# Kernel optimization log

Hardware: AMD Instinct MI355X
Metric: run time of the kernel (lower is better)

The kernel has to match this reference:

```python
import jax, jax.numpy as jnp
import numpy as np

N_ATOMS = 10000
N_PAIRS = 320000
C = 64        # channel width (pp_nodes[-1], ii_nodes[-1], pi_nodes[-1])
NB = 10       # n_basis
EPS = 1e-3    # torsion-boost epsilon


def setup_inputs() -> dict:
    key = jax.random.key(0)
    ks = jax.random.split(key, 24)
    f32 = jnp.float32

    def w(k, shp):
        return jax.random.normal(k, shp, f32) / np.float32(np.sqrt(shp[0]))

    ind_2 = jax.random.randint(ks[0], (N_PAIRS, 2), 0, N_ATOMS)
    p1 = jax.random.normal(ks[1], (N_ATOMS, C), f32)
    p3 = jax.random.normal(ks[2], (N_ATOMS, 3, C), f32)
    basis = jax.random.uniform(ks[3], (N_PAIRS, NB), dtype=f32)
    d3 = jax.random.normal(ks[4], (N_PAIRS, 3), f32)
    d3 = d3 / jnp.linalg.norm(d3, axis=-1, keepdims=True)  # unit bond directions
    fc_edge = jax.random.uniform(ks[5], (N_PAIRS, 1), dtype=f32)  # cutoff in [0,1]

    return {
        'ind_2': ind_2, 'p1': p1, 'p3': p3, 'basis': basis, 'd3': d3, 'fc_edge': fc_edge,
        'pp_pre_W1': w(ks[6], (C, C)), 'pp_pre_b1': jnp.zeros((C,), f32),
        'pp_pre_W2': w(ks[7], (C, C)), 'pp_pre_b2': jnp.zeros((C,), f32),
        'pi_W': w(ks[8], (2 * C, C * NB)), 'pi_b': jnp.zeros((C * NB,), f32),
        'ii_W': w(ks[9], (C, 2 * C)),
        'pp_post_W1': w(ks[10], (2 * C, C)), 'pp_post_W2': w(ks[11], (C, C)),
        'eq_pp_W': w(ks[12], (C, C)),
        'pp1_W1': w(ks[13], (2 * C, C)), 'pp1_b1': jnp.zeros((C,), f32),
        'pp1_W2': w(ks[14], (C, 2 * C)), 'pp1_b2': jnp.zeros((2 * C,), f32),
    }


def _gc_block(ind_2, p1, p3, basis, d3, fc_edge,
              pp_pre_W1, pp_pre_b1, pp_pre_W2, pp_pre_b2,
              pi_W, pi_b, ii_W, pp_post_W1, pp_post_W2,
              eq_pp_W, pp1_W1, pp1_b1, pp1_W2, pp1_b2):
    n_atoms = p1.shape[0]
    i = ind_2[:, 0]
    j = ind_2[:, 1]

    # ---- InvarLayer ----
    # pp_pre: FF [C,C], tanh, bias
    p1_in = jnp.tanh(jnp.tanh(p1 @ pp_pre_W1 + pp_pre_b1) @ pp_pre_W2 + pp_pre_b2)
    # PILayer: concat(p1[i], p1[j]) -> Dense(C*NB) -> contract with radial basis
    pair = jnp.concatenate([p1_in[i], p1_in[j]], axis=-1)            # (P, 2C)
    h = jnp.tanh(pair @ pi_W + pi_b).reshape(-1, C, NB)              # (P, C, NB)
    i_pair = jnp.einsum('pcb,pb->pc', h, basis)                      # (P, C)
    # ii: FF [2C] (doubled for n_props=2), tanh, no bias
    i_pair = jnp.tanh(i_pair @ ii_W)                                 # (P, 2C)
    # IP: scatter-add onto receiver atom i
    p1_scat = jax.ops.segment_sum(i_pair, i, num_segments=n_atoms)   # (N, 2C)
    # pp_post: FF [C,C], tanh, no bias
    p1_new = jnp.tanh(jnp.tanh(p1_scat @ pp_post_W1) @ pp_post_W2)   # (N, C)

    i1a, i1b = jnp.split(i_pair, 2, axis=-1)  # chunks; rank-3 branch uses i1s[1]

    # ---- torsion boost (compute_torsion_boost_t3) ----
    v = jax.ops.segment_sum(d3 * fc_edge, i, num_segments=n_atoms)   # (N, 3)
    v_i = v[i]
    proj = jnp.sum(v_i * d3, axis=-1, keepdims=True)
    w = v_i - proj * d3                                              # perpendicular part
    w2 = jnp.sum(w * w, axis=-1, keepdims=True)
    g_deg = w2 / (w2 + (10.0 * EPS) ** 2)
    t3 = w * jax.lax.rsqrt(w2 + EPS * EPS) * g_deg                   # (P, 3)
    tb_gate = g_deg * (fc_edge * fc_edge)                            # (P, 1)

    # ---- EquivarLayer ----
    gate = i1b[:, None, :]                                           # (P, 1, C)
    ix = p3[j] * gate + d3[:, :, None] * gate \
         + t3[:, :, None] * (i1b * tb_gate)[:, None, :]              # (P, 3, C)
    p3_new = jax.ops.segment_sum(ix, i, num_segments=n_atoms)        # (N, 3, C)
    p3_new = p3_new @ eq_pp_W                                        # PP: no bias, no act
    dotted = jnp.einsum('ixr,ixr->ir', p3_new, p3_new)               # (N, C)

    # ---- output PP + gating ----
    h2 = jnp.tanh(jnp.concatenate([p1_new, dotted], axis=-1) @ pp1_W1 + pp1_b1)
    h2 = jnp.tanh(h2 @ pp1_W2 + pp1_b2)                              # (N, 2C)
    g1, g3 = jnp.split(h2, 2, axis=-1)
    p1_out = g1                                                      # (N, C)
    p3_out = p3_new * g3[:, None, :]                                 # ScaleLayer
    return p1_out, p3_out


def reference(ind_2, p1, p3, basis, d3, fc_edge,
              pp_pre_W1, pp_pre_b1, pp_pre_W2, pp_pre_b2,
              pi_W, pi_b, ii_W, pp_post_W1, pp_post_W2,
              eq_pp_W, pp1_W1, pp1_b1, pp1_W2, pp1_b2):
    return _gc_block(ind_2, p1, p3, basis, d3, fc_edge,
                     pp_pre_W1, pp_pre_b1, pp_pre_W2, pp_pre_b2,
                     pi_W, pi_b, ii_W, pp_post_W1, pp_post_W2,
                     eq_pp_W, pp1_W1, pp1_b1, pp1_W2, pp1_b2)
```

## Files before the change

### kernel.cpp

```cpp
#include <hip/hip_runtime.h>
#include <hip/hip_bf16.h>

#define N_ATOMS 10000
#define N_PAIRS 320000
#define C_ 64
#define NB_ 10

typedef short bf16x8 __attribute__((ext_vector_type(8)));
typedef float f32x4 __attribute__((ext_vector_type(4)));

__device__ __forceinline__ float bf2f(__hip_bfloat16 x) { return __bfloat162float(x); }
__device__ __forceinline__ float ldf(const void* p, int i, int isf32) {
    return isf32 ? ((const float*)p)[i] : bf2f(((const __hip_bfloat16*)p)[i]);
}
__device__ __forceinline__ short f2bs(float x) {
    __hip_bfloat16 h = __float2bfloat16(x);
    return *reinterpret_cast<short*>(&h);
}
__device__ __forceinline__ float bs2f(unsigned short s) {
    return __uint_as_float(((unsigned)s) << 16);
}
__device__ __forceinline__ float tanh_fast(float x) {
    const float e = __expf(2.0f * x);
    return 1.0f - 2.0f * __builtin_amdgcn_rcpf(e + 1.0f);
}

#define W_PPREW1 0
#define W_PPREB1 4096
#define W_PPREW2 4160
#define W_PPREB2 8256
#define W_PIW    8320
#define W_PIB    90240
#define W_IIW    90880
#define W_PPOSTW1 99072
#define W_PPOSTW2 107264
#define W_EQW    111360
#define W_Q1W    115456
#define W_Q1B    123648
#define W_Q2W    123712
#define W_Q2B    131904
#define W_TOTAL  132032

__device__ __forceinline__ int probe_eval(const void* d3)
{
    float sf = 0.f, sb = 0.f;
    const float* f = (const float*)d3;
    const __hip_bfloat16* b = (const __hip_bfloat16*)d3;
    for (int r = 0; r < 4; r++) {
        float x = f[r*3], y = f[r*3+1], z = f[r*3+2];
        float n = x*x + y*y + z*z;
        sf += isfinite(n) ? fabsf(n - 1.f) : 1e30f;
        float xb = bf2f(b[r*3]), yb = bf2f(b[r*3+1]), zb = bf2f(b[r*3+2]);
        float nb = xb*xb + yb*yb + zb*zb;
        sb += isfinite(nb) ? fabsf(nb - 1.f) : 1e30f;
    }
    return (sf < sb) ? 1 : 0;
}

__global__ void k_probe(const void* __restrict__ d3, int* __restrict__ flag)
{
    if (threadIdx.x == 0 && blockIdx.x == 0) *flag = probe_eval(d3);
}

__global__ __launch_bounds__(256) void k_probe_hist_v(
    const void* __restrict__ d3, const void* __restrict__ fc,
    int* __restrict__ flag, const int* __restrict__ ind2,
    int* __restrict__ cnt, float* __restrict__ v)
{
    __shared__ int fsh;
    if (threadIdx.x == 0) {
        const int fv = probe_eval(d3);
        fsh = fv;
        if (blockIdx.x == 0) *flag = fv;
    }
    __syncthreads();
    const int isf32 = fsh;
    const int p = blockIdx.x * 256 + threadIdx.x;
    if (p >= N_PAIRS) return;
    const int ia = ind2[2 * p];
    atomicAdd(&cnt[ia], 1);
    const float f = ldf(fc, p, isf32);
    #pragma unroll
    for (int x = 0; x < 3; x++)
        atomicAdd(&v[ia * 3 + x], ldf(d3, 3 * p + x, isf32) * f);
}

__global__ __launch_bounds__(256) void k_convert_scan(
    const void* s0, const void* s1, const void* s2, const void* s3,
    const void* s4, const void* s5, const void* s6, const void* s7,
    const void* s8, const void* s9, const void* s10, const void* s11,
    const void* s12, const void* s13,
    float* __restrict__ wbuf, const int* __restrict__ flagp,
    const int* __restrict__ cnt, int* __restrict__ offs, int* __restrict__ cur)
{
    __shared__ int part[256];
    __shared__ int base[257];
    if (blockIdx.x < 516) {
        const int idx = blockIdx.x * 256 + threadIdx.x;
        if (idx >= W_TOTAL) return;
        const int isf32 = *flagp;
        const int offw[15] = {W_PPREW1, W_PPREB1, W_PPREW2, W_PPREB2, W_PIW, W_PIB,
                              W_IIW, W_PPOSTW1, W_PPOSTW2, W_EQW, W_Q1W, W_Q1B,
                              W_Q2W, W_Q2B, W_TOTAL};
        const void* srcs[14] = {s0,s1,s2,s3,s4,s5,s6,s7,s8,s9,s10,s11,s12,s13};
        int t = 0;
        while (idx >= offw[t + 1]) t++;
        wbuf[idx] = ldf(srcs[t], idx - offw[t], isf32);
        return;
    }
    const int t = threadIdx.x;
    const int lo = t * 40, hi = (lo + 40 < N_ATOMS) ? lo + 40 : N_ATOMS;
    int s = 0;
    for (int b = lo; b < hi; b++) s += cnt[b];
    part[t] = s;
    __syncthreads();
    if (t == 0) {
        int run = 0;
        for (int i = 0; i < 256; i++) { base[i] = run; run += part[i]; }
        base[256] = run;
    }
    __syncthreads();
    int run = base[t];
    for (int b = lo; b < hi; b++) { offs[b] = run; cur[b] = run; run += cnt[b]; }
    if (t == 0) offs[N_ATOMS] = base[256];
}

__global__ __launch_bounds__(256) void k_prep_scatter(
    const float* __restrict__ wbuf,
    short* __restrict__ piWB2,
    short* __restrict__ iiWh, short* __restrict__ iiWl,
    const void* __restrict__ p1, const int* __restrict__ flagp,
    unsigned short* __restrict__ p1h, unsigned short* __restrict__ p1l,
    const int* __restrict__ ind2, int* __restrict__ cur, int* __restrict__ perm)
{
    __shared__ float x[4][C_];
    __shared__ float h[4][C_];
    if (blockIdx.x >= 2852) {
        const int p = (blockIdx.x - 2852) * 256 + threadIdx.x;
        if (p < N_PAIRS) {
            const int pos = atomicAdd(&cur[ind2[2 * p]], 1);
            perm[pos] = p;
        }
        return;
    }
    if (blockIdx.x < 352) {
        int idx = blockIdx.x * 256 + threadIdx.x;
        if (idx < 81920) {
            const int j = idx & 7, lane = (idx >> 3) & 63, s = (idx >> 9) & 3, T = idx >> 11;
            const int k = s * 32 + (lane >> 4) * 8 + j;
            const int colp = T * 16 + (lane & 15);
            const int b = colp >> 6, c = colp & 63;
            const float v = wbuf[W_PIW + k * 640 + c * 10 + b];
            const short hs = f2bs(v);
            const int cc = idx >> 13, e = idx & 8191;
            piWB2[cc * 16384 + e] = hs;
            piWB2[cc * 16384 + 8192 + e] = f2bs(v - bs2f((unsigned short)hs));
            return;
        }
        idx -= 81920;
        if (idx < 8192) {
            const int j = idx & 7, lane = (idx >> 3) & 63, s2 = (idx >> 9) & 1, ct = idx >> 10;
            const int k = s2 * 32 + (lane >> 4) * 8 + j;
            const int col = ct * 16 + (lane & 15);
            const float wv = wbuf[W_IIW + k * 128 + col];
            const short hs = f2bs(wv);
            iiWh[idx] = hs;
            iiWl[idx] = f2bs(wv - bs2f((unsigned short)hs));
        }
        return;
    }
    const float* W1 = wbuf + W_PPREW1;
    const float* b1 = wbuf + W_PPREB1;
    const float* W2 = wbuf + W_PPREW2;
    const float* b2 = wbuf + W_PPREB2;
    const int isf32 = *flagp;
    const int t = threadIdx.x;
    const int slot = t >> 6, c = t & 63;
    const int atom = (blockIdx.x - 352) * 4 + slot;
    x[slot][c] = ldf(p1, atom * C_ + c, isf32);
    __syncthreads();
    float acc = b1[c];
    for (int k = 0; k < C_; k++) acc += x[slot][k] * W1[k * C_ + c];
    h[slot][c] = tanh_fast(acc);
    __syncthreads();
    acc = b2[c];
    for (int k = 0; k < C_; k++) acc += h[slot][k] * W2[k * C_ + c];
    const float f = tanh_fast(acc);
    const short hs = f2bs(f);
    p1h[atom * C_ + c] = (unsigned short)hs;
    p1l[atom * C_ + c] = (unsigned short)f2bs(f - bs2f((unsigned short)hs));
}

__global__ __launch_bounds__(256) void k_pairs_fused(
    const int* __restrict__ ind2, const void* __restrict__ basis,
    const void* __restrict__ d3, const void* __restrict__ fc,
    const int* __restrict__ perm,
    const void* __restrict__ p3,
    const float* __restrict__ wbuf,
    const short* __restrict__ piWB2,
    const short* __restrict__ iiWh, const short* __restrict__ iiWl,
    const unsigned short* __restrict__ p1h, const unsigned short* __restrict__ p1l,
    const int* __restrict__ flagp, const float* __restrict__ vglob,
    float* __restrict__ p1scat, float* __restrict__ p3acc)
{
    __shared__ __align__(16) char SH[33280];
    __shared__ float basisL[640];
    __shared__ float biasT[640];
    __shared__ int sIL[65], sJL[64];
    __shared__ float d3L[64][3], t3L[64][3], tbL[64];

    unsigned short* Bbuf = (unsigned short*)SH;
    float* preL = (float*)SH;
    float* ipL  = (float*)SH;

    const int t = threadIdx.x;
    const int bid = blockIdx.x;
    const int P0 = ((bid & 7) * 625 + (bid >> 3)) * 64;
    const int isf32 = *flagp;
    const int lane = t & 63;
    const int w = t >> 6;
    const int lc = lane & 15;
    const int quad = lane >> 4;

    if (t < 64) {
        const int p = perm[P0 + t];
        int2 ij = ((const int2*)ind2)[p];
        sIL[t] = ij.x; sJL[t] = ij.y;
        const float vi0 = vglob[ij.x * 3 + 0], vi1 = vglob[ij.x * 3 + 1], vi2 = vglob[ij.x * 3 + 2];
        const float d0 = ldf(d3, 3 * p + 0, isf32);
        const float d1 = ldf(d3, 3 * p + 1, isf32);
        const float d2 = ldf(d3, 3 * p + 2, isf32);
        d3L[t][0] = d0; d3L[t][1] = d1; d3L[t][2] = d2;
        const float proj = vi0 * d0 + vi1 * d1 + vi2 * d2;
        const float w0 = vi0 - proj * d0, w1 = vi1 - proj * d1, w2v = vi2 - proj * d2;
        const float w2 = w0 * w0 + w1 * w1 + w2v * w2v;
        const float g = w2 / (w2 + 1e-4f);
        const float rs = rsqrtf(w2 + 1e-6f);
        t3L[t][0] = w0 * rs * g; t3L[t][1] = w1 * rs * g; t3L[t][2] = w2v * rs * g;
        const float f = ldf(fc, p, isf32);
        tbL[t] = g * f * f;
    }
    if (t == 64) sIL[64] = -1;
    for (int e = t; e < 640; e += 256) {
        const int pm = e / 10, col = e - pm * 10;
        basisL[e] = ldf(basis, perm[P0 + pm] * 10 + col, isf32);
    }
    for (int e = t; e < 640; e += 256) biasT[e] = wbuf[W_PIB + (e & 63) * 10 + (e >> 6)];
    __syncthreads();

    bf16x8 ah[4], al[4];
    {
        const int ia = sIL[w * 16 + lc];
        const int ja = sJL[w * 16 + lc];
        #pragma unroll
        for (int s = 0; s < 4; s++) {
            const int atom = (s < 2) ? ia : ja;
            const int off = atom * 64 + (s & 1) * 32 + quad * 8;
            ah[s] = *(const bf16x8*)(p1h + off);
            al[s] = *(const bf16x8*)(p1l + off);
        }
    }

    float sr[4][4];
    #pragma unroll
    for (int r = 0; r < 4; r++)
        #pragma unroll
        for (int ph = 0; ph < 4; ph++) sr[r][ph] = 0.f;

    for (int cc = 0; cc < 10; cc++) {
        if (cc) __syncthreads();
        {
            const uint4* gsrc = (const uint4*)(piWB2 + cc * 16384);
            uint4* ldst = (uint4*)Bbuf;
            #pragma unroll
            for (int r = 0; r < 8; r++) ldst[r * 256 + t] = gsrc[r * 256 + t];
        }
        __syncthreads();
        #pragma unroll
        for (int tt = 0; tt < 4; tt++) {
            f32x4 acc = {0.f, 0.f, 0.f, 0.f};
            #pragma unroll
            for (int s = 0; s < 4; s++) {
                const int e = ((tt * 4 + s) * 64 + lane) * 8;
                bf16x8 bh = *(const bf16x8*)&Bbuf[e];
                bf16x8 bl = *(const bf16x8*)&Bbuf[8192 + e];
                acc = __builtin_amdgcn_mfma_f32_16x16x32_bf16(ah[s], bh, acc, 0, 0, 0);
                acc = __builtin_amdgcn_mfma_f32_16x16x32_bf16(al[s], bh, acc, 0, 0, 0);
                acc = __builtin_amdgcn_mfma_f32_16x16x32_bf16(ah[s], bl, acc, 0, 0, 0);
            }
            const float bias = biasT[cc * 64 + tt * 16 + lc];
            #pragma unroll
            for (int r = 0; r < 4; r++) {
                const int m = w * 16 + quad * 4 + r;
                const float h = tanh_fast(acc[r] + bias);
                sr[r][tt] += h * basisL[m * 10 + cc];
            }
        }
    }
    __syncthreads();

    #pragma unroll
    for (int r = 0; r < 4; r++)
        #pragma unroll
        for (int ph = 0; ph < 4; ph++)
            preL[(w * 16 + quad * 4 + r) * 68 + ph * 16 + lc] = sr[r][ph];
    __syncthreads();

    bf16x8 ah2[2], al2[2];
    {
        const int row = w * 16 + lc;
        #pragma unroll
        for (int s2 = 0; s2 < 2; s2++) {
            const float* pr2 = &preL[row * 68 + s2 * 32 + quad * 8];
            #pragma unroll
            for (int j = 0; j < 8; j++) {
                const float x = pr2[j];
                const short hs = f2bs(x);
                ah2[s2][j] = hs;
                al2[s2][j] = f2bs(x - bs2f((unsigned short)hs));
            }
        }
    }
    __syncthreads();

    float pv0[16];
    if (t < 192) {
        #pragma unroll
        for (int u = 0; u < 16; u++) pv0[u] = ldf(p3, sJL[u] * 192 + t, isf32);
    }

    #pragma unroll
    for (int ct = 0; ct < 8; ct++) {
        f32x4 acc = {0.f, 0.f, 0.f, 0.f};
        #pragma unroll
        for (int s2 = 0; s2 < 2; s2++) {
            bf16x8 bh = *(const bf16x8*)&iiWh[((ct * 2 + s2) * 64 + lane) * 8];
            bf16x8 bl = *(const bf16x8*)&iiWl[((ct * 2 + s2) * 64 + lane) * 8];
            acc = __builtin_amdgcn_mfma_f32_16x16x32_bf16(ah2[s2], bh, acc, 0, 0, 0);
            acc = __builtin_amdgcn_mfma_f32_16x16x32_bf16(al2[s2], bh, acc, 0, 0, 0);
            acc = __builtin_amdgcn_mfma_f32_16x16x32_bf16(ah2[s2], bl, acc, 0, 0, 0);
        }
        const int ch = ct * 16 + lc;
        #pragma unroll
        for (int r = 0; r < 4; r++) {
            const int m = w * 16 + quad * 4 + r;
            ipL[m * 130 + ch] = tanh_fast(acc[r]);
        }
    }
    __syncthreads();

    if (t < 192) {
        const int x = t >> 6, cc2 = t & 63;
        float acc = 0.f;
        #pragma unroll
        for (int blk = 0; blk < 4; blk++) {
            float pv[16];
            if (blk == 0) {
                #pragma unroll
                for (int u = 0; u < 16; u++) pv[u] = pv0[u];
            } else {
                #pragma unroll
                for (int u = 0; u < 16; u++)
                    pv[u] = ldf(p3, sJL[blk * 16 + u] * 192 + t, isf32);
            }
            #pragma unroll
            for (int u = 0; u < 16; u++) {
                const int m = blk * 16 + u;
                const float ipb = ipL[m * 130 + 64 + cc2];
                acc += (pv[u] + d3L[m][x]) * ipb + t3L[m][x] * (ipb * tbL[m]);
                if (sIL[m + 1] != sIL[m]) {
                    atomicAdd(&p3acc[(size_t)sIL[m] * 192 + t], acc);
                    acc = 0.f;
                }
            }
        }
    } else {
        const int ch0 = t - 192;
        float a0 = 0.f, a1 = 0.f;
        #pragma unroll 8
        for (int m = 0; m < 64; m++) {
            a0 += ipL[m * 130 + ch0];
            a1 += ipL[m * 130 + 64 + ch0];
            if (sIL[m + 1] != sIL[m]) {
                const size_t base = (size_t)sIL[m] * 128;
                atomicAdd(&p1scat[base + ch0], a0);
                atomicAdd(&p1scat[base + 64 + ch0], a1);
                a0 = 0.f; a1 = 0.f;
            }
        }
    }
}

__global__ __launch_bounds__(256) void k_pairs_atomic(
    const int* __restrict__ ind2, const void* __restrict__ basis,
    const void* __restrict__ d3, const void* __restrict__ fc,
    const void* __restrict__ p3,
    const float* __restrict__ wbuf,
    const short* __restrict__ piWB2,
    const short* __restrict__ iiWh, const short* __restrict__ iiWl,
    const unsigned short* __restrict__ p1h, const unsigned short* __restrict__ p1l,
    const int* __restrict__ flagp, const float* __restrict__ vglob,
    float* __restrict__ outA, float* __restrict__ outB)
{
    __shared__ __align__(16) unsigned short Bbuf[8192];
    __shared__ __align__(16) char SH[17408];
    __shared__ float basisL[640];
    __shared__ int sIL[64], sJL[64];
    __shared__ float d3L[64][3], t3L[64][3], tbL[64];

    float* preL = (float*)SH;
    float* i1bL = (float*)SH;

    const int t = threadIdx.x;
    const int P0 = blockIdx.x * 64;
    const int isf32 = *flagp;
    const int lane = t & 63;
    const int w = t >> 6;
    const int lc = lane & 15;
    const int quad = lane >> 4;

    if (t < 64) {
        int2 ij = ((const int2*)ind2)[P0 + t];
        sIL[t] = ij.x; sJL[t] = ij.y;
    }
    for (int e = t; e < 640; e += 256) basisL[e] = ldf(basis, P0 * 10 + e, isf32);
    __syncthreads();

    bf16x8 ah[4], al[4];
    {
        const int ia = sIL[w * 16 + lc];
        const int ja = sJL[w * 16 + lc];
        #pragma unroll
        for (int s = 0; s < 4; s++) {
            const int atom = (s < 2) ? ia : ja;
            const int off = atom * 64 + (s & 1) * 32 + quad * 8;
            ah[s] = *(const bf16x8*)(p1h + off);
            al[s] = *(const bf16x8*)(p1l + off);
        }
    }

    float sr[4][4];
    #pragma unroll
    for (int r = 0; r < 4; r++)
        #pragma unroll
        for (int ph = 0; ph < 4; ph++) sr[r][ph] = 0.f;

    for (int cc = 0; cc < 10; cc++) {
        f32x4 acc[4];
        #pragma unroll
        for (int tt = 0; tt < 4; tt++) acc[tt] = (f32x4){0.f, 0.f, 0.f, 0.f};

        __syncthreads();
        {
            const uint4* gsrc = (const uint4*)(piWB2 + cc * 16384);
            uint4* ldst = (uint4*)Bbuf;
            #pragma unroll
            for (int r = 0; r < 4; r++) ldst[r * 256 + t] = gsrc[r * 256 + t];
        }
        __syncthreads();
        #pragma unroll
        for (int tt = 0; tt < 4; tt++) {
            #pragma unroll
            for (int s = 0; s < 4; s++) {
                bf16x8 bfr = *(const bf16x8*)&Bbuf[((tt * 4 + s) * 64 + lane) * 8];
                acc[tt] = __builtin_amdgcn_mfma_f32_16x16x32_bf16(ah[s], bfr, acc[tt], 0, 0, 0);
                acc[tt] = __builtin_amdgcn_mfma_f32_16x16x32_bf16(al[s], bfr, acc[tt], 0, 0, 0);
            }
        }
        __syncthreads();
        {
            const uint4* gsrc = (const uint4*)(piWB2 + cc * 16384 + 8192);
            uint4* ldst = (uint4*)Bbuf;
            #pragma unroll
            for (int r = 0; r < 4; r++) ldst[r * 256 + t] = gsrc[r * 256 + t];
        }
        __syncthreads();
        #pragma unroll
        for (int tt = 0; tt < 4; tt++) {
            #pragma unroll
            for (int s = 0; s < 4; s++) {
                bf16x8 bfr = *(const bf16x8*)&Bbuf[((tt * 4 + s) * 64 + lane) * 8];
                acc[tt] = __builtin_amdgcn_mfma_f32_16x16x32_bf16(ah[s], bfr, acc[tt], 0, 0, 0);
            }
            const int c = tt * 16 + lc;
            const float bias = wbuf[W_PIB + c * 10 + cc];
            #pragma unroll
            for (int r = 0; r < 4; r++) {
                const int m = w * 16 + quad * 4 + r;
                const float h = tanh_fast(acc[tt][r] + bias);
                sr[r][tt] += h * basisL[m * 10 + cc];
            }
        }
    }

    #pragma unroll
    for (int r = 0; r < 4; r++)
        #pragma unroll
        for (int ph = 0; ph < 4; ph++)
            preL[(w * 16 + quad * 4 + r) * 68 + ph * 16 + lc] = sr[r][ph];
    __syncthreads();

    bf16x8 ah2[2], al2[2];
    {
        const int row = w * 16 + lc;
        #pragma unroll
        for (int s2 = 0; s2 < 2; s2++) {
            const float* pr2 = &preL[row * 68 + s2 * 32 + quad * 8];
            #pragma unroll
            for (int j = 0; j < 8; j++) {
                const float x = pr2[j];
                const short hs = f2bs(x);
                ah2[s2][j] = hs;
                al2[s2][j] = f2bs(x - bs2f((unsigned short)hs));
            }
        }
    }
    __syncthreads();

    #pragma unroll
    for (int ct = 0; ct < 8; ct++) {
        f32x4 acc = {0.f, 0.f, 0.f, 0.f};
        #pragma unroll
        for (int s2 = 0; s2 < 2; s2++) {
            bf16x8 bh = *(const bf16x8*)&iiWh[((ct * 2 + s2) * 64 + lane) * 8];
            bf16x8 bl = *(const bf16x8*)&iiWl[((ct * 2 + s2) * 64 + lane) * 8];
            acc = __builtin_amdgcn_mfma_f32_16x16x32_bf16(ah2[s2], bh, acc, 0, 0, 0);
            acc = __builtin_amdgcn_mfma_f32_16x16x32_bf16(al2[s2], bh, acc, 0, 0, 0);
            acc = __builtin_amdgcn_mfma_f32_16x16x32_bf16(ah2[s2], bl, acc, 0, 0, 0);
        }
        const int ch = ct * 16 + lc;
        #pragma unroll
        for (int r = 0; r < 4; r++) {
            const int m = w * 16 + quad * 4 + r;
            const float val = tanh_fast(acc[r]);
            atomicAdd(&outA[(size_t)sIL[m] * 128 + ch], val);
            if (ch >= 64) i1bL[m * 64 + (ch - 64)] = val;
        }
    }

    __syncthreads();
    if (t < 64) {
        const int m = t;
        const int ia = sIL[m];
        const float vi0 = vglob[ia * 3 + 0], vi1 = vglob[ia * 3 + 1], vi2 = vglob[ia * 3 + 2];
        const float d0 = ldf(d3, (P0 + m) * 3 + 0, isf32);
        const float d1 = ldf(d3, (P0 + m) * 3 + 1, isf32);
        const float d2 = ldf(d3, (P0 + m) * 3 + 2, isf32);
        d3L[m][0] = d0; d3L[m][1] = d1; d3L[m][2] = d2;
        const float proj = vi0 * d0 + vi1 * d1 + vi2 * d2;
        const float w0 = vi0 - proj * d0, w1 = vi1 - proj * d1, w2v = vi2 - proj * d2;
        const float w2 = w0 * w0 + w1 * w1 + w2v * w2v;
        const float g = w2 / (w2 + 1e-4f);
        const float rs = rsqrtf(w2 + 1e-6f);
        t3L[m][0] = w0 * rs * g; t3L[m][1] = w1 * rs * g; t3L[m][2] = w2v * rs * g;
        const float f = ldf(fc, P0 + m, isf32);
        tbL[m] = g * f * f;
    }
    __syncthreads();
    const int c = lane;
    #pragma unroll 4
    for (int mm = 0; mm < 16; mm++) {
        const int m = w * 16 + mm;
        const float bv = i1bL[m * 64 + c];
        const float coef = bv * tbL[m];
        #pragma unroll
        for (int x = 0; x < 3; x++) {
            const float p3v = ldf(p3, sJL[m] * 192 + x * 64 + c, isf32);
            atomicAdd(&outB[(size_t)sIL[m] * 192 + x * 64 + c],
                      p3v * bv + d3L[m][x] * bv + t3L[m][x] * coef);
        }
    }
}

__global__ __launch_bounds__(256) void k_final(
    const float* __restrict__ p1scat, const float* __restrict__ p3acc,
    const float* __restrict__ wbuf, const int* __restrict__ flagp,
    void* __restrict__ out)
{
    const float* ppW1 = wbuf + W_PPOSTW1;
    const float* ppW2 = wbuf + W_PPOSTW2;
    const float* eqW  = wbuf + W_EQW;
    const float* q1W  = wbuf + W_Q1W;
    const float* q1b  = wbuf + W_Q1B;
    const float* q2W  = wbuf + W_Q2W;
    const float* q2b  = wbuf + W_Q2B;
    const int isf32 = *flagp;

    __shared__ float s1[4][128];
    __shared__ float hA[4][64];
    __shared__ float cat[4][128];
    __shared__ float p3a[4][192];
    const int t = threadIdx.x;
    const int slot = t >> 6, c = t & 63;
    const int atom = blockIdx.x * 4 + slot;

    s1[slot][c]        = p1scat[atom * 128 + c];
    s1[slot][64 + c]   = p1scat[atom * 128 + 64 + c];
    p3a[slot][c]       = p3acc[atom * 192 + c];
    p3a[slot][64 + c]  = p3acc[atom * 192 + 64 + c];
    p3a[slot][128 + c] = p3acc[atom * 192 + 128 + c];
    __syncthreads();

    float acc = 0.f;
    for (int k = 0; k < 128; k++) acc += s1[slot][k] * ppW1[k * 64 + c];
    hA[slot][c] = tanh_fast(acc);
    __syncthreads();
    acc = 0.f;
    for (int k = 0; k < 64; k++) acc += hA[slot][k] * ppW2[k * 64 + c];
    cat[slot][c] = tanh_fast(acc);

    float pn[3];
    float dot = 0.f;
    #pragma unroll
    for (int x = 0; x < 3; x++) {
        float a = 0.f;
        for (int k = 0; k < 64; k++) a += p3a[slot][x * 64 + k] * eqW[k * 64 + c];
        pn[x] = a;
        dot += a * a;
    }
    cat[slot][64 + c] = dot;
    __syncthreads();

    acc = q1b[c];
    for (int k = 0; k < 128; k++) acc += cat[slot][k] * q1W[k * 64 + c];
    __syncthreads();
    hA[slot][c] = tanh_fast(acc);
    __syncthreads();

    float g1acc = q2b[c], g3acc = q2b[c + 64];
    for (int k = 0; k < 64; k++) {
        const float hv = hA[slot][k];
        g1acc += hv * q2W[k * 128 + c];
        g3acc += hv * q2W[k * 128 + c + 64];
    }
    const float g1 = tanh_fast(g1acc);
    const float g3 = tanh_fast(g3acc);
    if (isf32) {
        float* p1o = (float*)out;
        float* p3o = p1o + 640000;
        p1o[atom * 64 + c] = g1;
        #pragma unroll
        for (int x = 0; x < 3; x++) p3o[atom * 192 + x * 64 + c] = pn[x] * g3;
    } else {
        __hip_bfloat16* p1o = (__hip_bfloat16*)out;
        __hip_bfloat16* p3o = p1o + 640000;
        p1o[atom * 64 + c] = __float2bfloat16(g1);
        #pragma unroll
        for (int x = 0; x < 3; x++) p3o[atom * 192 + x * 64 + c] = __float2bfloat16(pn[x] * g3);
    }
}

__global__ __launch_bounds__(256) void k_vscat(
    const int* __restrict__ ind2, const void* __restrict__ d3,
    const void* __restrict__ fc, const int* __restrict__ flagp, float* __restrict__ v)
{
    const int p = blockIdx.x * 256 + threadIdx.x;
    if (p >= N_PAIRS) return;
    const int isf32 = *flagp;
    const int ia = ind2[2 * p];
    const float f = ldf(fc, p, isf32);
    atomicAdd(&v[ia * 3 + 0], ldf(d3, p * 3 + 0, isf32) * f);
    atomicAdd(&v[ia * 3 + 1], ldf(d3, p * 3 + 1, isf32) * f);
    atomicAdd(&v[ia * 3 + 2], ldf(d3, p * 3 + 2, isf32) * f);
}

extern "C" void kernel_launch(void* const* d_in, const int* in_sizes, int n_in,
                              void* d_out, int out_size, void* d_ws, size_t ws_size,
                              hipStream_t stream)
{
    const int* ind2 = (const int*)d_in[0];
    const void* p1    = d_in[1];
    const void* p3    = d_in[2];
    const void* basis = d_in[3];
    const void* d3    = d_in[4];
    const void* fc    = d_in[5];

    char* W = (char*)d_ws;
    float* wbuf  = (float*)(W + 0);
    short* piWB2 = (short*)(W + 528128);
    short* iiWh  = (short*)(W + 1183488);
    short* iiWl  = (short*)(W + 1199872);
    unsigned short* p1h = (unsigned short*)(W + 1216256);
    unsigned short* p1l = (unsigned short*)(W + 2496256);
    int* flag = (int*)(W + 3776256);

    const int fused = (ws_size >= 18096384ULL) ? 1 : 0;

    if (fused) {
        int* offs     = (int*)(W + 3776320);
        int* cur      = (int*)(W + 3816384);
        int* perm     = (int*)(W + 3856384);
        int* cnt      = (int*)(W + 5136384);
        float* v      = (float*)(W + 5176384);
        float* p1scat = (float*)(W + 5296384);
        float* p3acc  = (float*)(W + 10416384);

        hipMemsetAsync(cnt, 0, 40000 + 120000 + 5120000 + 7680000, stream);
        k_probe_hist_v<<<1250, 256, 0, stream>>>(d3, fc, flag, ind2, cnt, v);
        k_convert_scan<<<517, 256, 0, stream>>>(
            d_in[6], d_in[7], d_in[8], d_in[9], d_in[10], d_in[11], d_in[12],
            d_in[13], d_in[14], d_in[15], d_in[16], d_in[17], d_in[18], d_in[19],
            wbuf, flag, cnt, offs, cur);
        k_prep_scatter<<<4102, 256, 0, stream>>>(wbuf, piWB2, iiWh, iiWl, p1, flag,
                                                 p1h, p1l, ind2, cur, perm);
        k_pairs_fused<<<5000, 256, 0, stream>>>(ind2, basis, d3, fc, perm, p3,
                                                wbuf, piWB2, iiWh, iiWl,
                                                p1h, p1l, flag, v, p1scat, p3acc);
        k_final<<<2500, 256, 0, stream>>>(p1scat, p3acc, wbuf, flag, d_out);
    } else {
        float* v      = (float*)(W + 3776320);
        float* p1scat = (float*)(W + 3896320);
        float* p3acc  = (float*)(W + 9016320);

        hipMemsetAsync(v, 0, 120000 + 5120000 + 7680000, stream);
        k_probe<<<1, 64, 0, stream>>>(d3, flag);
        k_convert_scan<<<516, 256, 0, stream>>>(
            d_in[6], d_in[7], d_in[8], d_in[9], d_in[10], d_in[11], d_in[12],
            d_in[13], d_in[14], d_in[15], d_in[16], d_in[17], d_in[18], d_in[19],
            wbuf, flag, nullptr, nullptr, nullptr);
        k_prep_scatter<<<2852, 256, 0, stream>>>(wbuf, piWB2, iiWh, iiWl, p1, flag,
                                                 p1h, p1l, nullptr, nullptr, nullptr);
        k_vscat<<<1250, 256, 0, stream>>>(ind2, d3, fc, flag, v);
        k_pairs_atomic<<<5000, 256, 0, stream>>>(ind2, basis, d3, fc, p3,
                                                 wbuf, piWB2, iiWh, iiWl,
                                                 p1h, p1l, flag, v,
                                                 p1scat, p3acc);
        k_final<<<2500, 256, 0, stream>>>(p1scat, p3acc, wbuf, flag, d_out);
    }
}
```

Before: 516.1 us.

## Run pp_pre MLP with split-bf16 MFMA and merge front-end prep kernels

The per-atom pp_pre two-layer MLP now runs on MFMA 16x16x32 bf16 instructions, using a hi/lo split of inputs and weights (three products) to keep close to fp32 accuracy. This replaces the scalar loop that did one atom per 64 threads. The histogram/v-scatter and weight-conversion kernels are merged into one front kernel, and a small kernel now does the scan and builds the pp_pre weight fragments. The aim is to cut launch count and scalar FMA time in the prep stage, at the cost of an extra small launch and a new workspace layout.

```diff
diff --git a/kernel.cpp b/kernel.cpp
--- a/kernel.cpp
+++ b/kernel.cpp
@@ -57,15 +57,15 @@
     return (sf < sb) ? 1 : 0;
 }
 
-__global__ void k_probe(const void* __restrict__ d3, int* __restrict__ flag)
-{
-    if (threadIdx.x == 0 && blockIdx.x == 0) *flag = probe_eval(d3);
-}
-
-__global__ __launch_bounds__(256) void k_probe_hist_v(
+__global__ __launch_bounds__(256) void k_front(
     const void* __restrict__ d3, const void* __restrict__ fc,
     int* __restrict__ flag, const int* __restrict__ ind2,
-    int* __restrict__ cnt, float* __restrict__ v)
+    int* __restrict__ cnt, float* __restrict__ v,
+    const void* s0, const void* s1, const void* s2, const void* s3,
+    const void* s4, const void* s5, const void* s6, const void* s7,
+    const void* s8, const void* s9, const void* s10, const void* s11,
+    const void* s12, const void* s13,
+    float* __restrict__ wbuf)
 {
     __shared__ int fsh;
     if (threadIdx.x == 0) {
@@ -75,54 +75,67 @@
     }
     __syncthreads();
     const int isf32 = fsh;
-    const int p = blockIdx.x * 256 + threadIdx.x;
-    if (p >= N_PAIRS) return;
-    const int ia = ind2[2 * p];
-    atomicAdd(&cnt[ia], 1);
-    const float f = ldf(fc, p, isf32);
-    #pragma unroll
-    for (int x = 0; x < 3; x++)
-        atomicAdd(&v[ia * 3 + x], ldf(d3, 3 * p + x, isf32) * f);
-}
-
-__global__ __launch_bounds__(256) void k_convert_scan(
-    const void* s0, const void* s1, const void* s2, const void* s3,
-    const void* s4, const void* s5, const void* s6, const void* s7,
-    const void* s8, const void* s9, const void* s10, const void* s11,
-    const void* s12, const void* s13,
-    float* __restrict__ wbuf, const int* __restrict__ flagp,
-    const int* __restrict__ cnt, int* __restrict__ offs, int* __restrict__ cur)
+    if (blockIdx.x < 1250) {
+        const int p = blockIdx.x * 256 + threadIdx.x;
+        if (p >= N_PAIRS) return;
+        const int ia = ind2[2 * p];
+        atomicAdd(&cnt[ia], 1);
+        const float f = ldf(fc, p, isf32);
+        #pragma unroll
+        for (int x = 0; x < 3; x++)
+            atomicAdd(&v[ia * 3 + x], ldf(d3, 3 * p + x, isf32) * f);
+        return;
+    }
+    const int idx = (blockIdx.x - 1250) * 256 + threadIdx.x;
+    if (idx >= W_TOTAL) return;
+    const int offw[15] = {W_PPREW1, W_PPREB1, W_PPREW2, W_PPREB2, W_PIW, W_PIB,
+                          W_IIW, W_PPOSTW1, W_PPOSTW2, W_EQW, W_Q1W, W_Q1B,
+                          W_Q2W, W_Q2B, W_TOTAL};
+    const void* srcs[14] = {s0,s1,s2,s3,s4,s5,s6,s7,s8,s9,s10,s11,s12,s13};
+    int t = 0;
+    while (idx >= offw[t + 1]) t++;
+    wbuf[idx] = ldf(srcs[t], idx - offw[t], isf32);
+}
+
+__global__ __launch_bounds__(256) void k_scan_wfrag(
+    const int* __restrict__ cnt, int* __restrict__ offs, int* __restrict__ cur,
+    const float* __restrict__ wbuf,
+    short* __restrict__ w1Fh, short* __restrict__ w1Fl,
+    short* __restrict__ w2Fh, short* __restrict__ w2Fl)
 {
-    __shared__ int part[256];
-    __shared__ int base[257];
-    if (blockIdx.x < 516) {
-        const int idx = blockIdx.x * 256 + threadIdx.x;
-        if (idx >= W_TOTAL) return;
-        const int isf32 = *flagp;
-        const int offw[15] = {W_PPREW1, W_PPREB1, W_PPREW2, W_PPREB2, W_PIW, W_PIB,
-                              W_IIW, W_PPOSTW1, W_PPOSTW2, W_EQW, W_Q1W, W_Q1B,
-                              W_Q2W, W_Q2B, W_TOTAL};
-        const void* srcs[14] = {s0,s1,s2,s3,s4,s5,s6,s7,s8,s9,s10,s11,s12,s13};
-        int t = 0;
-        while (idx >= offw[t + 1]) t++;
-        wbuf[idx] = ldf(srcs[t], idx - offw[t], isf32);
+    if (blockIdx.x == 0) {
+        if (!cnt) return;
+        __shared__ int part[256];
+        __shared__ int base[257];
+        const int t = threadIdx.x;
+        const int lo = t * 40, hi = (lo + 40 < N_ATOMS) ? lo + 40 : N_ATOMS;
+        int s = 0;
+        for (int b = lo; b < hi; b++) s += cnt[b];
+        part[t] = s;
+        __syncthreads();
+        if (t == 0) {
+            int run = 0;
+            for (int i = 0; i < 256; i++) { base[i] = run; run += part[i]; }
+            base[256] = run;
+        }
+        __syncthreads();
+        int run = base[t];
+        for (int b = lo; b < hi; b++) { offs[b] = run; cur[b] = run; run += cnt[b]; }
+        if (t == 0) offs[N_ATOMS] = base[256];
         return;
     }
-    const int t = threadIdx.x;
-    const int lo = t * 40, hi = (lo + 40 < N_ATOMS) ? lo + 40 : N_ATOMS;
-    int s = 0;
-    for (int b = lo; b < hi; b++) s += cnt[b];
-    part[t] = s;
-    __syncthreads();
-    if (t == 0) {
-        int run = 0;
-        for (int i = 0; i < 256; i++) { base[i] = run; run += part[i]; }
-        base[256] = run;
-    }
-    __syncthreads();
-    int run = base[t];
-    for (int b = lo; b < hi; b++) { offs[b] = run; cur[b] = run; run += cnt[b]; }
-    if (t == 0) offs[N_ATOMS] = base[256];
+    const int b = blockIdx.x - 1;
+    const int isW2 = b >= 16;
+    const int idx = (b - (isW2 ? 16 : 0)) * 256 + threadIdx.x;
+    const int j = idx & 7, lane = (idx >> 3) & 63, s2 = (idx >> 9) & 1, ct = idx >> 10;
+    const int k = s2 * 32 + (lane >> 4) * 8 + j;
+    const int col = ct * 16 + (lane & 15);
+    const float wv = wbuf[(isW2 ? W_PPREW2 : W_PPREW1) + k * 64 + col];
+    const short hs = f2bs(wv);
+    short* dh = isW2 ? w2Fh : w1Fh;
+    short* dl = isW2 ? w2Fl : w1Fl;
+    dh[idx] = hs;
+    dl[idx] = f2bs(wv - bs2f((unsigned short)hs));
 }
 
 __global__ __launch_bounds__(256) void k_prep_scatter(
@@ -131,12 +144,13 @@
     short* __restrict__ iiWh, short* __restrict__ iiWl,
     const void* __restrict__ p1, const int* __restrict__ flagp,
     unsigned short* __restrict__ p1h, unsigned short* __restrict__ p1l,
-    const int* __restrict__ ind2, int* __restrict__ cur, int* __restrict__ perm)
+    const int* __restrict__ ind2, int* __restrict__ cur, int* __restrict__ perm,
+    const short* __restrict__ w1Fh, const short* __restrict__ w1Fl,
+    const short* __restrict__ w2Fh, const short* __restrict__ w2Fl)
 {
-    __shared__ float x[4][C_];
-    __shared__ float h[4][C_];
-    if (blockIdx.x >= 2852) {
-        const int p = (blockIdx.x - 2852) * 256 + threadIdx.x;
+    __shared__ float hL[64 * 68];
+    if (blockIdx.x >= 509) {
+        const int p = (blockIdx.x - 509) * 256 + threadIdx.x;
         if (p < N_PAIRS) {
             const int pos = atomicAdd(&cur[ind2[2 * p]], 1);
             perm[pos] = p;
@@ -169,26 +183,87 @@
         }
         return;
     }
-    const float* W1 = wbuf + W_PPREW1;
-    const float* b1 = wbuf + W_PPREB1;
-    const float* W2 = wbuf + W_PPREW2;
-    const float* b2 = wbuf + W_PPREB2;
     const int isf32 = *flagp;
     const int t = threadIdx.x;
-    const int slot = t >> 6, c = t & 63;
-    const int atom = (blockIdx.x - 352) * 4 + slot;
-    x[slot][c] = ldf(p1, atom * C_ + c, isf32);
-    __syncthreads();
-    float acc = b1[c];
-    for (int k = 0; k < C_; k++) acc += x[slot][k] * W1[k * C_ + c];
-    h[slot][c] = tanh_fast(acc);
-    __syncthreads();
-    acc = b2[c];
-    for (int k = 0; k < C_; k++) acc += h[slot][k] * W2[k * C_ + c];
-    const float f = tanh_fast(acc);
-    const short hs = f2bs(f);
-    p1h[atom * C_ + c] = (unsigned short)hs;
-    p1l[atom * C_ + c] = (unsigned short)f2bs(f - bs2f((unsigned short)hs));
+    const int lane = t & 63, w = t >> 6, lc = lane & 15, quad = lane >> 4;
+    const int B0 = (blockIdx.x - 352) * 64;
+
+    bf16x8 xh[2], xl[2];
+    {
+        const int a = B0 + w * 16 + lc;
+        const int ar = (a < N_ATOMS) ? a : N_ATOMS - 1;
+        #pragma unroll
+        for (int s2 = 0; s2 < 2; s2++) {
+            const int base = ar * 64 + s2 * 32 + quad * 8;
+            #pragma unroll
+            for (int j = 0; j < 8; j++) {
+                const float x = ldf(p1, base + j, isf32);
+                const short hs = f2bs(x);
+                xh[s2][j] = hs;
+                xl[s2][j] = f2bs(x - bs2f((unsigned short)hs));
+            }
+        }
+    }
+    #pragma unroll
+    for (int tt = 0; tt < 4; tt++) {
+        f32x4 acc = {0.f, 0.f, 0.f, 0.f};
+        #pragma unroll
+        for (int s2 = 0; s2 < 2; s2++) {
+            bf16x8 bh = *(const bf16x8*)&w1Fh[((tt * 2 + s2) * 64 + lane) * 8];
+            bf16x8 bl = *(const bf16x8*)&w1Fl[((tt * 2 + s2) * 64 + lane) * 8];
+            acc = __builtin_amdgcn_mfma_f32_16x16x32_bf16(xh[s2], bh, acc, 0, 0, 0);
+            acc = __builtin_amdgcn_mfma_f32_16x16x32_bf16(xl[s2], bh, acc, 0, 0, 0);
+            acc = __builtin_amdgcn_mfma_f32_16x16x32_bf16(xh[s2], bl, acc, 0, 0, 0);
+        }
+        const int c = tt * 16 + lc;
+        const float b1v = wbuf[W_PPREB1 + c];
+        #pragma unroll
+        for (int r = 0; r < 4; r++) {
+            const int m = w * 16 + quad * 4 + r;
+            hL[m * 68 + c] = tanh_fast(acc[r] + b1v);
+        }
+    }
+    __syncthreads();
+    bf16x8 hh[2], hl[2];
+    {
+        const int row = w * 16 + lc;
+        #pragma unroll
+        for (int s2 = 0; s2 < 2; s2++) {
+            const float* pr = &hL[row * 68 + s2 * 32 + quad * 8];
+            #pragma unroll
+            for (int j = 0; j < 8; j++) {
+                const float x = pr[j];
+                const short hs = f2bs(x);
+                hh[s2][j] = hs;
+                hl[s2][j] = f2bs(x - bs2f((unsigned short)hs));
+            }
+        }
+    }
+    #pragma unroll
+    for (int tt = 0; tt < 4; tt++) {
+        f32x4 acc = {0.f, 0.f, 0.f, 0.f};
+        #pragma unroll
+        for (int s2 = 0; s2 < 2; s2++) {
+            bf16x8 bh = *(const bf16x8*)&w2Fh[((tt * 2 + s2) * 64 + lane) * 8];
+            bf16x8 bl = *(const bf16x8*)&w2Fl[((tt * 2 + s2) * 64 + lane) * 8];
+            acc = __builtin_amdgcn_mfma_f32_16x16x32_bf16(hh[s2], bh, acc, 0, 0, 0);
+            acc = __builtin_amdgcn_mfma_f32_16x16x32_bf16(hl[s2], bh, acc, 0, 0, 0);
+            acc = __builtin_amdgcn_mfma_f32_16x16x32_bf16(hh[s2], bl, acc, 0, 0, 0);
+        }
+        const int c = tt * 16 + lc;
+        const float b2v = wbuf[W_PPREB2 + c];
+        #pragma unroll
+        for (int r = 0; r < 4; r++) {
+            const int m = w * 16 + quad * 4 + r;
+            const int a = B0 + m;
+            if (a < N_ATOMS) {
+                const float f = tanh_fast(acc[r] + b2v);
+                const short hs = f2bs(f);
+                p1h[a * 64 + c] = (unsigned short)hs;
+                p1l[a * 64 + c] = (unsigned short)f2bs(f - bs2f((unsigned short)hs));
+            }
+        }
+    }
 }
 
 __global__ __launch_bounds__(256) void k_pairs_fused(
@@ -650,20 +725,6 @@
     }
 }
 
-__global__ __launch_bounds__(256) void k_vscat(
-    const int* __restrict__ ind2, const void* __restrict__ d3,
-    const void* __restrict__ fc, const int* __restrict__ flagp, float* __restrict__ v)
-{
-    const int p = blockIdx.x * 256 + threadIdx.x;
-    if (p >= N_PAIRS) return;
-    const int isf32 = *flagp;
-    const int ia = ind2[2 * p];
-    const float f = ldf(fc, p, isf32);
-    atomicAdd(&v[ia * 3 + 0], ldf(d3, p * 3 + 0, isf32) * f);
-    atomicAdd(&v[ia * 3 + 1], ldf(d3, p * 3 + 1, isf32) * f);
-    atomicAdd(&v[ia * 3 + 2], ldf(d3, p * 3 + 2, isf32) * f);
-}
-
 extern "C" void kernel_launch(void* const* d_in, const int* in_sizes, int n_in,
                               void* d_out, int out_size, void* d_ws, size_t ws_size,
                               hipStream_t stream)
@@ -683,44 +744,52 @@
     unsigned short* p1h = (unsigned short*)(W + 1216256);
     unsigned short* p1l = (unsigned short*)(W + 2496256);
     int* flag = (int*)(W + 3776256);
-
-    const int fused = (ws_size >= 18096384ULL) ? 1 : 0;
+    short* w1Fh = (short*)(W + 3776320);
+    short* w1Fl = (short*)(W + 3784512);
+    short* w2Fh = (short*)(W + 3792704);
+    short* w2Fl = (short*)(W + 3800896);
+
+    const int fused = (ws_size >= 18129216ULL) ? 1 : 0;
 
     if (fused) {
-        int* offs     = (int*)(W + 3776320);
-        int* cur      = (int*)(W + 3816384);
-        int* perm     = (int*)(W + 3856384);
-        int* cnt      = (int*)(W + 5136384);
-        float* v      = (float*)(W + 5176384);
-        float* p1scat = (float*)(W + 5296384);
-        float* p3acc  = (float*)(W + 10416384);
+        int* offs     = (int*)(W + 3809088);
+        int* cur      = (int*)(W + 3849216);
+        int* perm     = (int*)(W + 3889216);
+        int* cnt      = (int*)(W + 5169216);
+        float* v      = (float*)(W + 5209216);
+        float* p1scat = (float*)(W + 5329216);
+        float* p3acc  = (float*)(W + 10449216);
 
         hipMemsetAsync(cnt, 0, 40000 + 120000 + 5120000 + 7680000, stream);
-        k_probe_hist_v<<<1250, 256, 0, stream>>>(d3, fc, flag, ind2, cnt, v);
-        k_convert_scan<<<517, 256, 0, stream>>>(
+        k_front<<<1766, 256, 0, stream>>>(d3, fc, flag, ind2, cnt, v,
             d_in[6], d_in[7], d_in[8], d_in[9], d_in[10], d_in[11], d_in[12],
             d_in[13], d_in[14], d_in[15], d_in[16], d_in[17], d_in[18], d_in[19],
-            wbuf, flag, cnt, offs, cur);
-        k_prep_scatter<<<4102, 256, 0, stream>>>(wbuf, piWB2, iiWh, iiWl, p1, flag,
-                                                 p1h, p1l, ind2, cur, perm);
+            wbuf);
+        k_scan_wfrag<<<33, 256, 0, stream>>>(cnt, offs, cur, wbuf,
+                                             w1Fh, w1Fl, w2Fh, w2Fl);
+        k_prep_scatter<<<1759, 256, 0, stream>>>(wbuf, piWB2, iiWh, iiWl, p1, flag,
+                                                 p1h, p1l, ind2, cur, perm,
+                                                 w1Fh, w1Fl, w2Fh, w2Fl);
         k_pairs_fused<<<5000, 256, 0, stream>>>(ind2, basis, d3, fc, perm, p3,
                                                 wbuf, piWB2, iiWh, iiWl,
                                                 p1h, p1l, flag, v, p1scat, p3acc);
         k_final<<<2500, 256, 0, stream>>>(p1scat, p3acc, wbuf, flag, d_out);
     } else {
-        float* v      = (float*)(W + 3776320);
-        float* p1scat = (float*)(W + 3896320);
-        float* p3acc  = (float*)(W + 9016320);
-
-        hipMemsetAsync(v, 0, 120000 + 5120000 + 7680000, stream);
-        k_probe<<<1, 64, 0, stream>>>(d3, flag);
-        k_convert_scan<<<516, 256, 0, stream>>>(
+        int* cnt      = (int*)(W + 3809088);
+        float* v      = (float*)(W + 3849088);
+        float* p1scat = (float*)(W + 3969088);
+        float* p3acc  = (float*)(W + 9089088);
+
+        hipMemsetAsync(cnt, 0, 40000 + 120000 + 5120000 + 7680000, stream);
+        k_front<<<1766, 256, 0, stream>>>(d3, fc, flag, ind2, cnt, v,
             d_in[6], d_in[7], d_in[8], d_in[9], d_in[10], d_in[11], d_in[12],
             d_in[13], d_in[14], d_in[15], d_in[16], d_in[17], d_in[18], d_in[19],
-            wbuf, flag, nullptr, nullptr, nullptr);
-        k_prep_scatter<<<2852, 256, 0, stream>>>(wbuf, piWB2, iiWh, iiWl, p1, flag,
-                                                 p1h, p1l, nullptr, nullptr, nullptr);
-        k_vscat<<<1250, 256, 0, stream>>>(ind2, d3, fc, flag, v);
+            wbuf);
+        k_scan_wfrag<<<33, 256, 0, stream>>>(nullptr, nullptr, nullptr, wbuf,
+                                             w1Fh, w1Fl, w2Fh, w2Fl);
+        k_prep_scatter<<<509, 256, 0, stream>>>(wbuf, piWB2, iiWh, iiWl, p1, flag,
+                                                p1h, p1l, nullptr, nullptr, nullptr,
+                                                w1Fh, w1Fl, w2Fh, w2Fl);
         k_pairs_atomic<<<5000, 256, 0, stream>>>(ind2, basis, d3, fc, p3,
                                                  wbuf, piWB2, iiWh, iiWl,
                                                  p1h, p1l, flag, v,
```

Measured after the change: 522.8 us. Within noise of the previous version (+1.3%).
